# Optimization experiments

Measured on AMD Instinct MI355X. Metric: run time of the kernel, lower is better.

The kernel has to match this reference:

```python
import jax, jax.numpy as jnp
import numpy as np

B, S, D = 4, 2048, 1024
H, DK, DV, DOUT = 16, 64, 64, 1024
NEG = -1.0e9


def setup_inputs() -> dict:
    key = jax.random.key(0)
    ks = jax.random.split(key, 12)
    sq = lambda fan_in: 1.0 / np.sqrt(fan_in)
    return {
        "query": jax.random.normal(ks[0], (B, S, D), jnp.float32),
        "key": jax.random.normal(ks[1], (B, S, D), jnp.float32),
        "value": jax.random.normal(ks[2], (B, S, D), jnp.float32),
        "attention_mask": jax.random.randint(ks[3], (B, 1, 1, S), 0, 2, jnp.int32),
        "wq": jax.random.normal(ks[4], (D, H * DK), jnp.float32) * sq(D),
        "bq": jnp.zeros((H * DK,), jnp.float32),
        "wk": jax.random.normal(ks[5], (D, H * DK), jnp.float32) * sq(D),
        "bk": jnp.zeros((H * DK,), jnp.float32),
        "wv": jax.random.normal(ks[6], (D, H * DV), jnp.float32) * sq(D),
        "bv": jnp.zeros((H * DV,), jnp.float32),
        "wo": jax.random.normal(ks[7], (H * DV, DOUT), jnp.float32) * sq(H * DV),
        "bo": jnp.zeros((DOUT,), jnp.float32),
    }


def _split_heads(x, head_dim):
    b, s, _ = x.shape
    return x.reshape(b, s, H, head_dim).transpose(0, 2, 1, 3)  # [B,H,S,hd]


def reference(query, key, value, attention_mask, wq, bq, wk, bk, wv, bv, wo, bo):
    q = _split_heads(query @ wq + bq, DK)   # [B,H,S,DK]
    k = _split_heads(key @ wk + bk, DK)     # [B,H,S,DK]
    v = _split_heads(value @ wv + bv, DV)   # [B,H,S,DV]
    logits = jnp.einsum("bhqd,bhkd->bhqk", q, k) / jnp.sqrt(jnp.float32(DK))
    logits = logits + attention_mask.astype(logits.dtype) * NEG
    attn = jax.nn.softmax(logits, axis=-1)
    out = jnp.einsum("bhqk,bhkd->bhqd", attn, v)          # [B,H,S,DV]
    out = out.transpose(0, 2, 1, 3).reshape(query.shape[0], -1, H * DV)
    return out @ wo + bo
```

## Files before the change

### kernel.cpp

```cpp
#include <hip/hip_runtime.h>
#include <hip/hip_bf16.h>
#include <math.h>

#define Bv 4
#define Sv 2048
#define Dv 1024
#define Hv 16
#define HD 64
#define NEGV (-1.0e9f)

typedef __attribute__((ext_vector_type(8))) short bf16x8;
typedef __attribute__((ext_vector_type(4))) short s16x4;
typedef __attribute__((ext_vector_type(4))) float f32x4;

__device__ __forceinline__ short f2bf(float f) {
    union { __hip_bfloat16 h; short s; } u;
    u.h = __float2bfloat16(f);
    return u.s;
}

#if __has_builtin(__builtin_amdgcn_exp2f)
#define EXP2F(x) __builtin_amdgcn_exp2f(x)
#else
#define EXP2F(x) __expf((x) * 0.6931471805599453f)
#endif

__device__ __forceinline__ void glds16(const void* g, void* l) {
    __builtin_amdgcn_global_load_lds(
        (const __attribute__((address_space(1))) void*)g,
        (__attribute__((address_space(3))) void*)l, 16, 0, 0);
}

__global__ __launch_bounds__(256) void cvt_bf16(const float* __restrict__ X,
                                                unsigned short* __restrict__ Y) {
    const size_t i = ((size_t)blockIdx.x * 256 + threadIdx.x) * 8;
    const float4 a = *(const float4*)&X[i];
    const float4 b = *(const float4*)&X[i + 4];
    bf16x8 o = {f2bf(a.x), f2bf(a.y), f2bf(a.z), f2bf(a.w),
                f2bf(b.x), f2bf(b.y), f2bf(b.z), f2bf(b.w)};
    *(bf16x8*)&Y[i] = o;
}

__global__ __launch_bounds__(256) void transpose_w(const float* __restrict__ W,
                                                   unsigned short* __restrict__ WT) {
    __shared__ float T[64][65];
    const int t = threadIdx.x;
    const int n0 = blockIdx.x * 64, k0 = blockIdx.y * 64;
    #pragma unroll
    for (int i = 0; i < 4; ++i) {
        const int k = (t >> 4) + 16 * i;
        const int nc = (t & 15) * 4;
        const float4 v = *(const float4*)&W[(size_t)(k0 + k) * 1024 + n0 + nc];
        T[k][nc + 0] = v.x; T[k][nc + 1] = v.y;
        T[k][nc + 2] = v.z; T[k][nc + 3] = v.w;
    }
    __syncthreads();
    const int n = t >> 2, kc = (t & 3) * 16;
    #pragma unroll
    for (int j4 = 0; j4 < 4; ++j4) {
        s16x4 o;
        #pragma unroll
        for (int jj = 0; jj < 4; ++jj) o[jj] = f2bf(T[kc + j4 * 4 + jj][n]);
        *(s16x4*)&WT[(size_t)(n0 + n) * 1024 + k0 + kc + j4 * 4] = o;
    }
}

__global__ __launch_bounds__(256) void transpose_v(const unsigned short* __restrict__ Vin,
                                                   unsigned short* __restrict__ VT) {
    __shared__ unsigned short T[64][72];
    const int t = threadIdx.x;
    const int s0 = blockIdx.x * 64;
    const int bh = blockIdx.y;
    const size_t ib = (size_t)bh * Sv * 64;
    const size_t ob = (size_t)bh * 64 * Sv;
    {
        const int s = t >> 2, dc = (t & 3) * 16;
        const bf16x8 a = *(const bf16x8*)&Vin[ib + (size_t)(s0 + s) * 64 + dc];
        const bf16x8 b = *(const bf16x8*)&Vin[ib + (size_t)(s0 + s) * 64 + dc + 8];
        *(bf16x8*)&T[s][dc] = a;
        *(bf16x8*)&T[s][dc + 8] = b;
    }
    __syncthreads();
    const int dv = t >> 2, sc = (t & 3) * 16;
    #pragma unroll
    for (int j4 = 0; j4 < 4; ++j4) {
        s16x4 o;
        #pragma unroll
        for (int jj = 0; jj < 4; ++jj) o[jj] = (short)T[sc + j4 * 4 + jj][dv];
        *(s16x4*)&VT[ob + (size_t)dv * Sv + s0 + sc + j4 * 4] = o;
    }
}

template <int PERM>
__global__ __launch_bounds__(256) void gemm_mfma(const unsigned short* __restrict__ X,
                                                 const unsigned short* __restrict__ WT,
                                                 const float* __restrict__ bias,
                                                 void* __restrict__ Cv,
                                                 int M, int N, int K) {
    __shared__ short As[128 * 32];
    __shared__ short Bs[128 * 32];

    const int t = threadIdx.x;
    const int lane = t & 63, w = t >> 6;
    const int l15 = lane & 15, quad = lane >> 4;
    const int m0 = blockIdx.y * 128, n0 = blockIdx.x * 128;
    const int wm = (w >> 1) * 64, wn = (w & 1) * 64;

    f32x4 acc[4][4];
    #pragma unroll
    for (int mi = 0; mi < 4; ++mi)
        #pragma unroll
        for (int ni = 0; ni < 4; ++ni) acc[mi][ni] = (f32x4){0.f, 0.f, 0.f, 0.f};

    const int srow = lane >> 2;
    const int skc = (lane & 3) * 8;

    for (int k0 = 0; k0 < K; k0 += 32) {
        #pragma unroll
        for (int i = 0; i < 2; ++i) {
            const int seg = w * 2 + i;
            const int row = seg * 16 + srow;
            glds16(&WT[(size_t)(n0 + row) * K + k0 + skc], &Bs[seg * 512]);
            glds16(&X[(size_t)(m0 + row) * K + k0 + skc], &As[seg * 512]);
        }
        __syncthreads();

        bf16x8 afr[4], bfr[4];
        #pragma unroll
        for (int mi = 0; mi < 4; ++mi)
            afr[mi] = *(const bf16x8*)&As[(wm + mi * 16 + l15) * 32 + quad * 8];
        #pragma unroll
        for (int ni = 0; ni < 4; ++ni)
            bfr[ni] = *(const bf16x8*)&Bs[(wn + ni * 16 + l15) * 32 + quad * 8];
        #pragma unroll
        for (int mi = 0; mi < 4; ++mi)
            #pragma unroll
            for (int ni = 0; ni < 4; ++ni)
                acc[mi][ni] = __builtin_amdgcn_mfma_f32_16x16x32_bf16(
                    afr[mi], bfr[ni], acc[mi][ni], 0, 0, 0);
        __syncthreads();
    }

    #pragma unroll
    for (int mi = 0; mi < 4; ++mi) {
        #pragma unroll
        for (int ni = 0; ni < 4; ++ni) {
            const int col = n0 + wn + ni * 16 + l15;
            const float bsv = bias[col];
            #pragma unroll
            for (int r = 0; r < 4; ++r) {
                const int row = m0 + wm + mi * 16 + quad * 4 + r;
                const float vv = acc[mi][ni][r] + bsv;
                if constexpr (PERM == 0) {
                    ((float*)Cv)[(size_t)row * N + col] = vv;
                } else {
                    const int bb = row / Sv, s = row % Sv;
                    const int hh = col >> 6, d = col & 63;
                    ((unsigned short*)Cv)[((((size_t)bb * Hv + hh) * Sv + s) << 6) + d] =
                        (unsigned short)f2bf(vv);
                }
            }
        }
    }
}

__global__ __launch_bounds__(256, 4) void attn_mfma(const unsigned short* __restrict__ Q,
                                                    const unsigned short* __restrict__ Kg,
                                                    const unsigned short* __restrict__ VT,
                                                    const int* __restrict__ mask,
                                                    unsigned short* __restrict__ O) {
    __shared__ short Kl[64 * 72];
    __shared__ short Vl[64 * 72];
    __shared__ short Sl[128 * 72];
    __shared__ float Mk[64];

    const int t = threadIdx.x;
    const int lane = t & 63, w = t >> 6;
    const int l15 = lane & 15, quad = lane >> 4;
    const int q0 = blockIdx.x * 128;
    const int h = blockIdx.y, b = blockIdx.z;
    const int bh = b * Hv + h;
    const size_t kvb = (size_t)bh * Sv * 64;
    const size_t vtb = (size_t)bh * 64 * Sv;

    bf16x8 qf[2][2];
    #pragma unroll
    for (int ni = 0; ni < 2; ++ni) {
        const size_t qa = kvb + (size_t)(q0 + w * 32 + ni * 16 + l15) * 64 + quad * 8;
        qf[ni][0] = *(const bf16x8*)&Q[qa];
        qf[ni][1] = *(const bf16x8*)&Q[qa + 32];
    }

    float l_acc[2] = {0.f, 0.f};
    f32x4 oacc[2][4];
    #pragma unroll
    for (int mi = 0; mi < 2; ++mi)
        #pragma unroll
        for (int ni = 0; ni < 4; ++ni) oacc[mi][ni] = (f32x4){0.f, 0.f, 0.f, 0.f};

    const int srow = t >> 2, sch = (t & 3) * 16;
    const unsigned short* Kst = Kg + kvb + (size_t)srow * 64 + sch;
    const unsigned short* Vst = VT + vtb + (size_t)srow * Sv + sch;
    const int* Mst = mask + (size_t)b * Sv;

    bf16x8 kr0 = *(const bf16x8*)&Kst[0];
    bf16x8 kr1 = *(const bf16x8*)&Kst[8];
    bf16x8 vr0 = *(const bf16x8*)&Vst[0];
    bf16x8 vr1 = *(const bf16x8*)&Vst[8];
    int mreg = (t < 64) ? Mst[t] : 0;

    constexpr float CS = 0.18033688011112042f;
    constexpr float CM = NEGV * 1.4426950408889634f;

    for (int k0 = 0; k0 < Sv; k0 += 64) {
        __syncthreads();
        *(bf16x8*)&Kl[srow * 72 + sch] = kr0;
        *(bf16x8*)&Kl[srow * 72 + sch + 8] = kr1;
        *(bf16x8*)&Vl[srow * 72 + sch] = vr0;
        *(bf16x8*)&Vl[srow * 72 + sch + 8] = vr1;
        if (t < 64) Mk[t] = CM * (float)mreg;
        __syncthreads();

        if (k0 + 64 < Sv) {
            kr0 = *(const bf16x8*)&Kst[(size_t)(k0 + 64) * 64];
            kr1 = *(const bf16x8*)&Kst[(size_t)(k0 + 64) * 64 + 8];
            vr0 = *(const bf16x8*)&Vst[k0 + 64];
            vr1 = *(const bf16x8*)&Vst[k0 + 64 + 8];
            if (t < 64) mreg = Mst[k0 + 64 + t];
        }

        #pragma unroll
        for (int mi = 0; mi < 4; ++mi) {
            const bf16x8 kf0 = *(const bf16x8*)&Kl[(mi * 16 + l15) * 72 + quad * 8];
            const bf16x8 kf1 = *(const bf16x8*)&Kl[(mi * 16 + l15) * 72 + 32 + quad * 8];
            const float4 mk4 = *(const float4*)&Mk[mi * 16 + quad * 4];
            #pragma unroll
            for (int ni = 0; ni < 2; ++ni) {
                f32x4 st = (f32x4){0.f, 0.f, 0.f, 0.f};
                st = __builtin_amdgcn_mfma_f32_16x16x32_bf16(kf0, qf[ni][0], st, 0, 0, 0);
                st = __builtin_amdgcn_mfma_f32_16x16x32_bf16(kf1, qf[ni][1], st, 0, 0, 0);
                const float p0 = EXP2F(__builtin_fmaf(st[0], CS, mk4.x));
                const float p1 = EXP2F(__builtin_fmaf(st[1], CS, mk4.y));
                const float p2 = EXP2F(__builtin_fmaf(st[2], CS, mk4.z));
                const float p3 = EXP2F(__builtin_fmaf(st[3], CS, mk4.w));
                l_acc[ni] += (p0 + p1) + (p2 + p3);
                s16x4 pv = {f2bf(p0), f2bf(p1), f2bf(p2), f2bf(p3)};
                *(s16x4*)&Sl[(w * 32 + ni * 16 + l15) * 72 + mi * 16 + quad * 4] = pv;
            }
        }

        bf16x8 vf[4][2];
        #pragma unroll
        for (int ni = 0; ni < 4; ++ni) {
            vf[ni][0] = *(const bf16x8*)&Vl[(ni * 16 + l15) * 72 + quad * 8];
            vf[ni][1] = *(const bf16x8*)&Vl[(ni * 16 + l15) * 72 + 32 + quad * 8];
        }

        #pragma unroll
        for (int mi = 0; mi < 2; ++mi) {
            const bf16x8 pf0 = *(const bf16x8*)&Sl[(w * 32 + mi * 16 + l15) * 72 + quad * 8];
            const bf16x8 pf1 = *(const bf16x8*)&Sl[(w * 32 + mi * 16 + l15) * 72 + 32 + quad * 8];
            #pragma unroll
            for (int ni = 0; ni < 4; ++ni) {
                oacc[mi][ni] = __builtin_amdgcn_mfma_f32_16x16x32_bf16(pf0, vf[ni][0], oacc[mi][ni], 0, 0, 0);
                oacc[mi][ni] = __builtin_amdgcn_mfma_f32_16x16x32_bf16(pf1, vf[ni][1], oacc[mi][ni], 0, 0, 0);
            }
        }
    }

    #pragma unroll
    for (int mi = 0; mi < 2; ++mi) {
        float l = l_acc[mi];
        l += __shfl_xor(l, 16);
        l += __shfl_xor(l, 32);
        #pragma unroll
        for (int r = 0; r < 4; ++r) {
            const float lr = __shfl(l, quad * 4 + r, 64);
            const float inv = 1.0f / lr;
            const size_t row = (size_t)b * Sv + q0 + w * 32 + mi * 16 + quad * 4 + r;
            #pragma unroll
            for (int ni = 0; ni < 4; ++ni) {
                O[row * (Hv * HD) + h * HD + ni * 16 + l15] =
                    (unsigned short)f2bf(oacc[mi][ni][r] * inv);
            }
        }
    }
}

extern "C" void kernel_launch(void* const* d_in, const int* in_sizes, int n_in,
                              void* d_out, int out_size, void* d_ws, size_t ws_size,
                              hipStream_t stream) {
    const float* query = (const float*)d_in[0];
    const float* key   = (const float*)d_in[1];
    const float* value = (const float*)d_in[2];
    const int*   amask = (const int*)d_in[3];
    const float* wq = (const float*)d_in[4];
    const float* bq = (const float*)d_in[5];
    const float* wk = (const float*)d_in[6];
    const float* bk = (const float*)d_in[7];
    const float* wv = (const float*)d_in[8];
    const float* bv = (const float*)d_in[9];
    const float* wo = (const float*)d_in[10];
    const float* bo = (const float*)d_in[11];
    float* out = (float*)d_out;

    unsigned short* wsp = (unsigned short*)d_ws;
    dim3 bb(256), gt(16, 16);

    if (ws_size >= (size_t)64 * 1024 * 1024) {
        const size_t PBQ = (size_t)Bv * Hv * Sv * HD;
        unsigned short* qb = wsp;
        unsigned short* kb = qb + PBQ;
        unsigned short* vb = kb + PBQ;
        unsigned short* ab = vb + PBQ;
        unsigned short* wt_kb = kb;
        unsigned short* wt_out = (unsigned short*)d_out;
        unsigned short* wt_vb = vb;

        const int M = Bv * Sv;
        dim3 gg(8, M / 128), gc(M * 1024 / 2048);

        cvt_bf16<<<gc, bb, 0, stream>>>(value, ab);
        transpose_w<<<gt, bb, 0, stream>>>(wv, wt_kb);
        gemm_mfma<1><<<gg, bb, 0, stream>>>(ab, wt_kb, bv, qb, M, 1024, 1024);
        transpose_v<<<dim3(Sv / 64, Bv * Hv), bb, 0, stream>>>(qb, vb);

        cvt_bf16<<<gc, bb, 0, stream>>>(query, ab);
        transpose_w<<<gt, bb, 0, stream>>>(wq, wt_kb);
        gemm_mfma<1><<<gg, bb, 0, stream>>>(ab, wt_kb, bq, qb, M, 1024, 1024);

        cvt_bf16<<<gc, bb, 0, stream>>>(key, ab);
        transpose_w<<<gt, bb, 0, stream>>>(wk, wt_out);
        gemm_mfma<1><<<gg, bb, 0, stream>>>(ab, wt_out, bk, kb, M, 1024, 1024);

        attn_mfma<<<dim3(Sv / 128, Hv, Bv), bb, 0, stream>>>(qb, kb, vb, amask, ab);

        transpose_w<<<gt, bb, 0, stream>>>(wo, wt_vb);
        gemm_mfma<0><<<gg, bb, 0, stream>>>(ab, wt_vb, bo, out, M, 1024, 1024);
    } else {
        const size_t PQ = (size_t)Hv * Sv * HD;
        unsigned short* qb = wsp;
        unsigned short* kb = qb + PQ;
        unsigned short* vb = kb + PQ;
        unsigned short* ab = vb + PQ;
        const int M = Sv;
        dim3 gg(8, M / 128), gc(M * 1024 / 2048);
        for (int b = 0; b < Bv; ++b) {
            const size_t xoff = (size_t)b * Sv * Dv;
            unsigned short* wt_kb = kb;
            unsigned short* wt_out = (unsigned short*)(out + xoff);
            unsigned short* wt_vb = vb;

            cvt_bf16<<<gc, bb, 0, stream>>>(value + xoff, ab);
            transpose_w<<<gt, bb, 0, stream>>>(wv, wt_kb);
            gemm_mfma<1><<<gg, bb, 0, stream>>>(ab, wt_kb, bv, qb, M, 1024, 1024);
            transpose_v<<<dim3(Sv / 64, Hv), bb, 0, stream>>>(qb, vb);

            cvt_bf16<<<gc, bb, 0, stream>>>(query + xoff, ab);
            transpose_w<<<gt, bb, 0, stream>>>(wq, wt_kb);
            gemm_mfma<1><<<gg, bb, 0, stream>>>(ab, wt_kb, bq, qb, M, 1024, 1024);

            cvt_bf16<<<gc, bb, 0, stream>>>(key + xoff, ab);
            transpose_w<<<gt, bb, 0, stream>>>(wk, wt_out);
            gemm_mfma<1><<<gg, bb, 0, stream>>>(ab, wt_out, bk, kb, M, 1024, 1024);

            attn_mfma<<<dim3(Sv / 128, Hv, 1), bb, 0, stream>>>(qb, kb, vb,
                                                                amask + (size_t)b * Sv, ab);

            transpose_w<<<gt, bb, 0, stream>>>(wo, wt_vb);
            gemm_mfma<0><<<gg, bb, 0, stream>>>(ab, wt_vb, bo, out + xoff, M, 1024, 1024);
        }
    }
}
```

Measured before the change: 412.4 us.

## Switch attention to 32x32 MFMA with register-resident P and swizzled LDS

Rewrites the attention kernel to use 32x32x16 bf16 MFMA tiles, computing S^T so that the exponentiated probabilities land in registers already in the A-operand layout for the PV MFMA. This removes the shared-memory round trip for P and its buffer. It also replaces padded K/V LDS rows with an XOR swizzle to avoid bank conflicts. The register layout change risks higher register pressure and occupancy loss, and the V fragment is read with split 8-byte loads.

Result: slower. 487.7 us (+18.2%).

```diff
diff --git a/kernel.cpp b/kernel.cpp
--- a/kernel.cpp
+++ b/kernel.cpp
@@ -12,11 +12,18 @@
 typedef __attribute__((ext_vector_type(8))) short bf16x8;
 typedef __attribute__((ext_vector_type(4))) short s16x4;
 typedef __attribute__((ext_vector_type(4))) float f32x4;
+typedef __attribute__((ext_vector_type(16))) float f32x16;
 
 __device__ __forceinline__ short f2bf(float f) {
     union { __hip_bfloat16 h; short s; } u;
     u.h = __float2bfloat16(f);
     return u.s;
+}
+
+__device__ __forceinline__ unsigned pkbf(float a, float b) {
+    union { __hip_bfloat162 h2; unsigned u; } un;
+    un.h2 = __float22bfloat162_rn(make_float2(a, b));
+    return un.u;
 }
 
 #if __has_builtin(__builtin_amdgcn_exp2f)
@@ -169,38 +176,40 @@
                                                     const unsigned short* __restrict__ VT,
                                                     const int* __restrict__ mask,
                                                     unsigned short* __restrict__ O) {
-    __shared__ short Kl[64 * 72];
-    __shared__ short Vl[64 * 72];
-    __shared__ short Sl[128 * 72];
+    __shared__ short Kl[64 * 64];
+    __shared__ short Vl[64 * 64];
     __shared__ float Mk[64];
 
     const int t = threadIdx.x;
     const int lane = t & 63, w = t >> 6;
-    const int l15 = lane & 15, quad = lane >> 4;
+    const int l31 = lane & 31, hi = lane >> 5;
     const int q0 = blockIdx.x * 128;
     const int h = blockIdx.y, b = blockIdx.z;
     const int bh = b * Hv + h;
     const size_t kvb = (size_t)bh * Sv * 64;
     const size_t vtb = (size_t)bh * 64 * Sv;
-
-    bf16x8 qf[2][2];
-    #pragma unroll
-    for (int ni = 0; ni < 2; ++ni) {
-        const size_t qa = kvb + (size_t)(q0 + w * 32 + ni * 16 + l15) * 64 + quad * 8;
-        qf[ni][0] = *(const bf16x8*)&Q[qa];
-        qf[ni][1] = *(const bf16x8*)&Q[qa + 32];
-    }
-
-    float l_acc[2] = {0.f, 0.f};
-    f32x4 oacc[2][4];
-    #pragma unroll
-    for (int mi = 0; mi < 2; ++mi)
-        #pragma unroll
-        for (int ni = 0; ni < 4; ++ni) oacc[mi][ni] = (f32x4){0.f, 0.f, 0.f, 0.f};
-
-    const int srow = t >> 2, sch = (t & 3) * 16;
-    const unsigned short* Kst = Kg + kvb + (size_t)srow * 64 + sch;
-    const unsigned short* Vst = VT + vtb + (size_t)srow * Sv + sch;
+    const int fsw = (l31 & 7) << 4;
+
+    bf16x8 qf[4];
+    {
+        const unsigned short* Qb = Q + kvb + (size_t)(q0 + w * 32 + l31) * 64;
+        #pragma unroll
+        for (int j = 0; j < 4; ++j) qf[j] = *(const bf16x8*)&Qb[j * 16 + hi * 8];
+    }
+
+    float l_acc = 0.f;
+    f32x16 oacc[2];
+    #pragma unroll
+    for (int d = 0; d < 2; ++d)
+        #pragma unroll
+        for (int i = 0; i < 16; ++i) oacc[d][i] = 0.f;
+
+    const int srow = t >> 2;
+    const int ssw = (srow & 7) << 4;
+    const int sc0 = ((t & 3) * 32) ^ ssw;
+    const int sc1 = ((t & 3) * 32 + 16) ^ ssw;
+    const unsigned short* Kst = Kg + kvb + (size_t)srow * 64 + (t & 3) * 16;
+    const unsigned short* Vst = VT + vtb + (size_t)srow * Sv + (t & 3) * 16;
     const int* Mst = mask + (size_t)b * Sv;
 
     bf16x8 kr0 = *(const bf16x8*)&Kst[0];
@@ -214,10 +223,10 @@
 
     for (int k0 = 0; k0 < Sv; k0 += 64) {
         __syncthreads();
-        *(bf16x8*)&Kl[srow * 72 + sch] = kr0;
-        *(bf16x8*)&Kl[srow * 72 + sch + 8] = kr1;
-        *(bf16x8*)&Vl[srow * 72 + sch] = vr0;
-        *(bf16x8*)&Vl[srow * 72 + sch + 8] = vr1;
+        *(bf16x8*)((char*)Kl + srow * 128 + sc0) = kr0;
+        *(bf16x8*)((char*)Kl + srow * 128 + sc1) = kr1;
+        *(bf16x8*)((char*)Vl + srow * 128 + sc0) = vr0;
+        *(bf16x8*)((char*)Vl + srow * 128 + sc1) = vr1;
         if (t < 64) Mk[t] = CM * (float)mreg;
         __syncthreads();
 
@@ -229,60 +238,66 @@
             if (t < 64) mreg = Mst[k0 + 64 + t];
         }
 
-        #pragma unroll
-        for (int mi = 0; mi < 4; ++mi) {
-            const bf16x8 kf0 = *(const bf16x8*)&Kl[(mi * 16 + l15) * 72 + quad * 8];
-            const bf16x8 kf1 = *(const bf16x8*)&Kl[(mi * 16 + l15) * 72 + 32 + quad * 8];
-            const float4 mk4 = *(const float4*)&Mk[mi * 16 + quad * 4];
-            #pragma unroll
-            for (int ni = 0; ni < 2; ++ni) {
-                f32x4 st = (f32x4){0.f, 0.f, 0.f, 0.f};
-                st = __builtin_amdgcn_mfma_f32_16x16x32_bf16(kf0, qf[ni][0], st, 0, 0, 0);
-                st = __builtin_amdgcn_mfma_f32_16x16x32_bf16(kf1, qf[ni][1], st, 0, 0, 0);
-                const float p0 = EXP2F(__builtin_fmaf(st[0], CS, mk4.x));
-                const float p1 = EXP2F(__builtin_fmaf(st[1], CS, mk4.y));
-                const float p2 = EXP2F(__builtin_fmaf(st[2], CS, mk4.z));
-                const float p3 = EXP2F(__builtin_fmaf(st[3], CS, mk4.w));
-                l_acc[ni] += (p0 + p1) + (p2 + p3);
-                s16x4 pv = {f2bf(p0), f2bf(p1), f2bf(p2), f2bf(p3)};
-                *(s16x4*)&Sl[(w * 32 + ni * 16 + l15) * 72 + mi * 16 + quad * 4] = pv;
-            }
-        }
-
-        bf16x8 vf[4][2];
-        #pragma unroll
-        for (int ni = 0; ni < 4; ++ni) {
-            vf[ni][0] = *(const bf16x8*)&Vl[(ni * 16 + l15) * 72 + quad * 8];
-            vf[ni][1] = *(const bf16x8*)&Vl[(ni * 16 + l15) * 72 + 32 + quad * 8];
-        }
-
-        #pragma unroll
-        for (int mi = 0; mi < 2; ++mi) {
-            const bf16x8 pf0 = *(const bf16x8*)&Sl[(w * 32 + mi * 16 + l15) * 72 + quad * 8];
-            const bf16x8 pf1 = *(const bf16x8*)&Sl[(w * 32 + mi * 16 + l15) * 72 + 32 + quad * 8];
-            #pragma unroll
-            for (int ni = 0; ni < 4; ++ni) {
-                oacc[mi][ni] = __builtin_amdgcn_mfma_f32_16x16x32_bf16(pf0, vf[ni][0], oacc[mi][ni], 0, 0, 0);
-                oacc[mi][ni] = __builtin_amdgcn_mfma_f32_16x16x32_bf16(pf1, vf[ni][1], oacc[mi][ni], 0, 0, 0);
-            }
-        }
-    }
-
-    #pragma unroll
-    for (int mi = 0; mi < 2; ++mi) {
-        float l = l_acc[mi];
-        l += __shfl_xor(l, 16);
-        l += __shfl_xor(l, 32);
-        #pragma unroll
-        for (int r = 0; r < 4; ++r) {
-            const float lr = __shfl(l, quad * 4 + r, 64);
-            const float inv = 1.0f / lr;
-            const size_t row = (size_t)b * Sv + q0 + w * 32 + mi * 16 + quad * 4 + r;
-            #pragma unroll
-            for (int ni = 0; ni < 4; ++ni) {
-                O[row * (Hv * HD) + h * HD + ni * 16 + l15] =
-                    (unsigned short)f2bf(oacc[mi][ni][r] * inv);
-            }
+        bf16x8 paf[2][2];
+        #pragma unroll
+        for (int kb = 0; kb < 2; ++kb) {
+            f32x16 st;
+            #pragma unroll
+            for (int i = 0; i < 16; ++i) st[i] = 0.f;
+            #pragma unroll
+            for (int j = 0; j < 4; ++j) {
+                const bf16x8 kf = *(const bf16x8*)((const char*)Kl +
+                    (kb * 32 + l31) * 128 + ((j * 32 + hi * 16) ^ fsw));
+                st = __builtin_amdgcn_mfma_f32_32x32x16_bf16(kf, qf[j], st, 0, 0, 0);
+            }
+            float p[16];
+            #pragma unroll
+            for (int g = 0; g < 4; ++g) {
+                const float4 mk4 = *(const float4*)&Mk[kb * 32 + 8 * g + 4 * hi];
+                const float e0 = EXP2F(__builtin_fmaf(st[4 * g + 0], CS, mk4.x));
+                const float e1 = EXP2F(__builtin_fmaf(st[4 * g + 1], CS, mk4.y));
+                const float e2 = EXP2F(__builtin_fmaf(st[4 * g + 2], CS, mk4.z));
+                const float e3 = EXP2F(__builtin_fmaf(st[4 * g + 3], CS, mk4.w));
+                p[4 * g + 0] = e0; p[4 * g + 1] = e1;
+                p[4 * g + 2] = e2; p[4 * g + 3] = e3;
+                l_acc += (e0 + e1) + (e2 + e3);
+            }
+            #pragma unroll
+            for (int ks = 0; ks < 2; ++ks) {
+                union { unsigned u[4]; bf16x8 v; } pu;
+                #pragma unroll
+                for (int wd = 0; wd < 4; ++wd)
+                    pu.u[wd] = pkbf(p[8 * ks + 2 * wd], p[8 * ks + 2 * wd + 1]);
+                paf[kb][ks] = pu.v;
+            }
+        }
+
+        #pragma unroll
+        for (int db = 0; db < 2; ++db) {
+            const char* vrow = (const char*)Vl + (db * 32 + l31) * 128;
+            #pragma unroll
+            for (int js = 0; js < 4; ++js) {
+                const int bofs = js * 32 + hi * 8;
+                union { s16x4 h[2]; bf16x8 v; } vu;
+                vu.h[0] = *(const s16x4*)(vrow + (bofs ^ fsw));
+                vu.h[1] = *(const s16x4*)(vrow + ((bofs + 16) ^ fsw));
+                oacc[db] = __builtin_amdgcn_mfma_f32_32x32x16_bf16(
+                    paf[js >> 1][js & 1], vu.v, oacc[db], 0, 0, 0);
+            }
+        }
+    }
+
+    float l = l_acc + __shfl_xor(l_acc, 32);
+    const float linv = 1.0f / l;
+    #pragma unroll
+    for (int db = 0; db < 2; ++db) {
+        #pragma unroll
+        for (int r = 0; r < 16; ++r) {
+            const int rowl = (r & 3) + 8 * (r >> 2) + 4 * hi;
+            const float inv = __shfl(linv, rowl, 64);
+            const size_t row = (size_t)b * Sv + q0 + w * 32 + rowl;
+            O[row * (Hv * HD) + h * HD + db * 32 + l31] =
+                (unsigned short)f2bf(oacc[db][r] * inv);
         }
     }
 }
```

## Fuse QKV projections into one launch with in-kernel fp32-to-bf16 conversion

Applied to the files above, without the earlier changes.

Replaces the separate cvt/transpose/gemm launches with a single batched weight-transpose kernel, one fused QKV GEMM that reads fp32 activations and converts them to bf16 while staging into LDS, and writes V directly in transposed layout, which removes transpose_v. Attention writes its output in head-major layout in place over Q, and a new output GEMM gathers from that layout. The aim is to cut launch count, the intermediate bf16 activation round trips and the extra V transpose pass. In exchange, the A operand now goes through register loads and conversion instead of async LDS loads, which may expose latency, and the scattered V-transposed stores are uncoalesced.

Result: faster. 394.3 us (-4.4%).

```diff
diff --git a/kernel.cpp b/kernel.cpp
--- a/kernel.cpp
+++ b/kernel.cpp
@@ -41,8 +41,8 @@
     *(bf16x8*)&Y[i] = o;
 }
 
-__global__ __launch_bounds__(256) void transpose_w(const float* __restrict__ W,
-                                                   unsigned short* __restrict__ WT) {
+__device__ __forceinline__ void transpose_w_body(const float* __restrict__ W,
+                                                 unsigned short* __restrict__ WT) {
     __shared__ float T[64][65];
     const int t = threadIdx.x;
     const int n0 = blockIdx.x * 64, k0 = blockIdx.y * 64;
@@ -63,6 +63,21 @@
         for (int jj = 0; jj < 4; ++jj) o[jj] = f2bf(T[kc + j4 * 4 + jj][n]);
         *(s16x4*)&WT[(size_t)(n0 + n) * 1024 + k0 + kc + j4 * 4] = o;
     }
+}
+
+__global__ __launch_bounds__(256) void transpose_w(const float* __restrict__ W,
+                                                   unsigned short* __restrict__ WT) {
+    transpose_w_body(W, WT);
+}
+
+__global__ __launch_bounds__(256) void transpose_w4(const float* __restrict__ W0,
+                                                    const float* __restrict__ W1,
+                                                    const float* __restrict__ W2,
+                                                    const float* __restrict__ W3,
+                                                    unsigned short* __restrict__ WTb) {
+    const int z = blockIdx.z;
+    const float* W = (z == 0) ? W0 : (z == 1) ? W1 : (z == 2) ? W2 : W3;
+    transpose_w_body(W, WTb + (size_t)z * 1048576);
 }
 
 __global__ __launch_bounds__(256) void transpose_v(const unsigned short* __restrict__ Vin,
@@ -164,6 +179,172 @@
     }
 }
 
+__global__ __launch_bounds__(256) void gemm_qkv(const float* __restrict__ Xq,
+                                                const float* __restrict__ Xk,
+                                                const float* __restrict__ Xv,
+                                                const unsigned short* __restrict__ WTb,
+                                                const float* __restrict__ bq,
+                                                const float* __restrict__ bk,
+                                                const float* __restrict__ bv,
+                                                unsigned short* __restrict__ Oq,
+                                                unsigned short* __restrict__ Ok,
+                                                unsigned short* __restrict__ Ov) {
+    __shared__ short As[128 * 32];
+    __shared__ short Bs[128 * 32];
+
+    const int hw = blockIdx.x + 8 * (blockIdx.y + 64 * blockIdx.z);
+    const int wl = (hw & 7) * 192 + (hw >> 3);
+    const int bx = wl & 7, by = (wl >> 3) & 63, bz = wl >> 9;
+
+    const float* X = (bz == 0) ? Xq : (bz == 1) ? Xk : Xv;
+    const unsigned short* WT = WTb + (size_t)bz * 1048576;
+    const float* bias = (bz == 0) ? bq : (bz == 1) ? bk : bv;
+
+    const int t = threadIdx.x;
+    const int lane = t & 63, w = t >> 6;
+    const int l15 = lane & 15, quad = lane >> 4;
+    const int m0 = by * 128, n0 = bx * 128;
+    const int wm = (w >> 1) * 64, wn = (w & 1) * 64;
+
+    f32x4 acc[4][4];
+    #pragma unroll
+    for (int mi = 0; mi < 4; ++mi)
+        #pragma unroll
+        for (int ni = 0; ni < 4; ++ni) acc[mi][ni] = (f32x4){0.f, 0.f, 0.f, 0.f};
+
+    const int srow = lane >> 2;
+    const int skc = (lane & 3) * 8;
+
+    for (int k0 = 0; k0 < 1024; k0 += 32) {
+        float4 fa[2][2];
+        #pragma unroll
+        for (int i = 0; i < 2; ++i) {
+            const int seg = w * 2 + i;
+            const int row = seg * 16 + srow;
+            glds16(&WT[(size_t)(n0 + row) * 1024 + k0 + skc], &Bs[seg * 512]);
+            const float* src = &X[(size_t)(m0 + row) * 1024 + k0 + skc];
+            fa[i][0] = *(const float4*)src;
+            fa[i][1] = *(const float4*)(src + 4);
+        }
+        #pragma unroll
+        for (int i = 0; i < 2; ++i) {
+            const int seg = w * 2 + i;
+            bf16x8 o = {f2bf(fa[i][0].x), f2bf(fa[i][0].y), f2bf(fa[i][0].z), f2bf(fa[i][0].w),
+                        f2bf(fa[i][1].x), f2bf(fa[i][1].y), f2bf(fa[i][1].z), f2bf(fa[i][1].w)};
+            *(bf16x8*)&As[seg * 512 + lane * 8] = o;
+        }
+        __syncthreads();
+
+        bf16x8 afr[4], bfr[4];
+        #pragma unroll
+        for (int mi = 0; mi < 4; ++mi)
+            afr[mi] = *(const bf16x8*)&As[(wm + mi * 16 + l15) * 32 + quad * 8];
+        #pragma unroll
+        for (int ni = 0; ni < 4; ++ni)
+            bfr[ni] = *(const bf16x8*)&Bs[(wn + ni * 16 + l15) * 32 + quad * 8];
+        #pragma unroll
+        for (int mi = 0; mi < 4; ++mi)
+            #pragma unroll
+            for (int ni = 0; ni < 4; ++ni)
+                acc[mi][ni] = __builtin_amdgcn_mfma_f32_16x16x32_bf16(
+                    afr[mi], bfr[ni], acc[mi][ni], 0, 0, 0);
+        __syncthreads();
+    }
+
+    #pragma unroll
+    for (int mi = 0; mi < 4; ++mi) {
+        #pragma unroll
+        for (int ni = 0; ni < 4; ++ni) {
+            const int col = n0 + wn + ni * 16 + l15;
+            const float bsv = bias[col];
+            const int hh = col >> 6, d = col & 63;
+            #pragma unroll
+            for (int r = 0; r < 4; ++r) {
+                const int row = m0 + wm + mi * 16 + quad * 4 + r;
+                const int bb = row >> 11, s = row & 2047;
+                const unsigned short v = (unsigned short)f2bf(acc[mi][ni][r] + bsv);
+                if (bz == 2) {
+                    Ov[((((size_t)bb * Hv + hh) * 64 + d) << 11) + s] = v;
+                } else {
+                    unsigned short* O = (bz == 0) ? Oq : Ok;
+                    O[((((size_t)bb * Hv + hh) * Sv + s) << 6) + d] = v;
+                }
+            }
+        }
+    }
+}
+
+__global__ __launch_bounds__(256) void gemm_out(const unsigned short* __restrict__ Xp,
+                                                const unsigned short* __restrict__ WT,
+                                                const float* __restrict__ bias,
+                                                float* __restrict__ C) {
+    __shared__ short As[128 * 32];
+    __shared__ short Bs[128 * 32];
+
+    const int hw = blockIdx.x + 8 * blockIdx.y;
+    const int wl = (hw & 7) * 64 + (hw >> 3);
+    const int bx = wl & 7, by = wl >> 3;
+
+    const int t = threadIdx.x;
+    const int lane = t & 63, w = t >> 6;
+    const int l15 = lane & 15, quad = lane >> 4;
+    const int m0 = by * 128, n0 = bx * 128;
+    const int wm = (w >> 1) * 64, wn = (w & 1) * 64;
+
+    f32x4 acc[4][4];
+    #pragma unroll
+    for (int mi = 0; mi < 4; ++mi)
+        #pragma unroll
+        for (int ni = 0; ni < 4; ++ni) acc[mi][ni] = (f32x4){0.f, 0.f, 0.f, 0.f};
+
+    const int srow = lane >> 2;
+    const int skc = (lane & 3) * 8;
+
+    for (int k0 = 0; k0 < 1024; k0 += 32) {
+        const int hh = k0 >> 6, db = (k0 & 63);
+        #pragma unroll
+        for (int i = 0; i < 2; ++i) {
+            const int seg = w * 2 + i;
+            const int row = seg * 16 + srow;
+            glds16(&WT[(size_t)(n0 + row) * 1024 + k0 + skc], &Bs[seg * 512]);
+            const int rb = m0 + row;
+            const int bb = rb >> 11, s = rb & 2047;
+            glds16(&Xp[((((size_t)bb * Hv + hh) * Sv + s) << 6) + db + skc], &As[seg * 512]);
+        }
+        __syncthreads();
+
+        bf16x8 afr[4], bfr[4];
+        #pragma unroll
+        for (int mi = 0; mi < 4; ++mi)
+            afr[mi] = *(const bf16x8*)&As[(wm + mi * 16 + l15) * 32 + quad * 8];
+        #pragma unroll
+        for (int ni = 0; ni < 4; ++ni)
+            bfr[ni] = *(const bf16x8*)&Bs[(wn + ni * 16 + l15) * 32 + quad * 8];
+        #pragma unroll
+        for (int mi = 0; mi < 4; ++mi)
+            #pragma unroll
+            for (int ni = 0; ni < 4; ++ni)
+                acc[mi][ni] = __builtin_amdgcn_mfma_f32_16x16x32_bf16(
+                    afr[mi], bfr[ni], acc[mi][ni], 0, 0, 0);
+        __syncthreads();
+    }
+
+    #pragma unroll
+    for (int mi = 0; mi < 4; ++mi) {
+        #pragma unroll
+        for (int ni = 0; ni < 4; ++ni) {
+            const int col = n0 + wn + ni * 16 + l15;
+            const float bsv = bias[col];
+            #pragma unroll
+            for (int r = 0; r < 4; ++r) {
+                const int row = m0 + wm + mi * 16 + quad * 4 + r;
+                C[(size_t)row * 1024 + col] = acc[mi][ni][r] + bsv;
+            }
+        }
+    }
+}
+
+template <int OL>
 __global__ __launch_bounds__(256, 4) void attn_mfma(const unsigned short* __restrict__ Q,
                                                     const unsigned short* __restrict__ Kg,
                                                     const unsigned short* __restrict__ VT,
@@ -277,11 +458,15 @@
         for (int r = 0; r < 4; ++r) {
             const float lr = __shfl(l, quad * 4 + r, 64);
             const float inv = 1.0f / lr;
-            const size_t row = (size_t)b * Sv + q0 + w * 32 + mi * 16 + quad * 4 + r;
+            const int s = q0 + w * 32 + mi * 16 + quad * 4 + r;
             #pragma unroll
             for (int ni = 0; ni < 4; ++ni) {
-                O[row * (Hv * HD) + h * HD + ni * 16 + l15] =
-                    (unsigned short)f2bf(oacc[mi][ni][r] * inv);
+                const unsigned short v = (unsigned short)f2bf(oacc[mi][ni][r] * inv);
+                if constexpr (OL == 0) {
+                    O[((size_t)b * Sv + s) * (Hv * HD) + h * HD + ni * 16 + l15] = v;
+                } else {
+                    O[kvb + ((size_t)s << 6) + ni * 16 + l15] = v;
+                }
             }
         }
     }
@@ -305,7 +490,7 @@
     float* out = (float*)d_out;
 
     unsigned short* wsp = (unsigned short*)d_ws;
-    dim3 bb(256), gt(16, 16);
+    dim3 bb(256);
 
     if (ws_size >= (size_t)64 * 1024 * 1024) {
         const size_t PBQ = (size_t)Bv * Hv * Sv * HD;
@@ -313,30 +498,15 @@
         unsigned short* kb = qb + PBQ;
         unsigned short* vb = kb + PBQ;
         unsigned short* ab = vb + PBQ;
-        unsigned short* wt_kb = kb;
-        unsigned short* wt_out = (unsigned short*)d_out;
-        unsigned short* wt_vb = vb;
-
-        const int M = Bv * Sv;
-        dim3 gg(8, M / 128), gc(M * 1024 / 2048);
-
-        cvt_bf16<<<gc, bb, 0, stream>>>(value, ab);
-        transpose_w<<<gt, bb, 0, stream>>>(wv, wt_kb);
-        gemm_mfma<1><<<gg, bb, 0, stream>>>(ab, wt_kb, bv, qb, M, 1024, 1024);
-        transpose_v<<<dim3(Sv / 64, Bv * Hv), bb, 0, stream>>>(qb, vb);
-
-        cvt_bf16<<<gc, bb, 0, stream>>>(query, ab);
-        transpose_w<<<gt, bb, 0, stream>>>(wq, wt_kb);
-        gemm_mfma<1><<<gg, bb, 0, stream>>>(ab, wt_kb, bq, qb, M, 1024, 1024);
-
-        cvt_bf16<<<gc, bb, 0, stream>>>(key, ab);
-        transpose_w<<<gt, bb, 0, stream>>>(wk, wt_out);
-        gemm_mfma<1><<<gg, bb, 0, stream>>>(ab, wt_out, bk, kb, M, 1024, 1024);
-
-        attn_mfma<<<dim3(Sv / 128, Hv, Bv), bb, 0, stream>>>(qb, kb, vb, amask, ab);
-
-        transpose_w<<<gt, bb, 0, stream>>>(wo, wt_vb);
-        gemm_mfma<0><<<gg, bb, 0, stream>>>(ab, wt_vb, bo, out, M, 1024, 1024);
+
+        transpose_w4<<<dim3(16, 16, 4), bb, 0, stream>>>(wq, wk, wv, wo, ab);
+
+        gemm_qkv<<<dim3(8, 64, 3), bb, 0, stream>>>(query, key, value, ab,
+                                                    bq, bk, bv, qb, kb, vb);
+
+        attn_mfma<1><<<dim3(Sv / 128, Hv, Bv), bb, 0, stream>>>(qb, kb, vb, amask, qb);
+
+        gemm_out<<<dim3(8, 64), bb, 0, stream>>>(qb, ab + (size_t)3 * 1048576, bo, out);
     } else {
         const size_t PQ = (size_t)Hv * Sv * HD;
         unsigned short* qb = wsp;
@@ -344,7 +514,7 @@
         unsigned short* vb = kb + PQ;
         unsigned short* ab = vb + PQ;
         const int M = Sv;
-        dim3 gg(8, M / 128), gc(M * 1024 / 2048);
+        dim3 gg(8, M / 128), gc(M * 1024 / 2048), gt(16, 16);
         for (int b = 0; b < Bv; ++b) {
             const size_t xoff = (size_t)b * Sv * Dv;
             unsigned short* wt_kb = kb;
@@ -364,8 +534,8 @@
             transpose_w<<<gt, bb, 0, stream>>>(wk, wt_out);
             gemm_mfma<1><<<gg, bb, 0, stream>>>(ab, wt_out, bk, kb, M, 1024, 1024);
 
-            attn_mfma<<<dim3(Sv / 128, Hv, 1), bb, 0, stream>>>(qb, kb, vb,
-                                                                amask + (size_t)b * Sv, ab);
+            attn_mfma<0><<<dim3(Sv / 128, Hv, 1), bb, 0, stream>>>(qb, kb, vb,
+                                                                   amask + (size_t)b * Sv, ab);
 
             transpose_w<<<gt, bb, 0, stream>>>(wo, wt_vb);
             gemm_mfma<0><<<gg, bb, 0, stream>>>(ab, wt_vb, bo, out + xoff, M, 1024, 1024);
```
